# Kernel optimization log

Measured on AMD Instinct MI355X. Metric: run time of the kernel, lower is better.

## Reference

```python
import jax, jax.numpy as jnp
import numpy as np

HEAD_DIM = 128
BAND_BITS = (5, 4, 4, 3)
N_BANDS = len(BAND_BITS)
BAND = HEAD_DIM // N_BANDS  # 32
FP16_MAX = 65504.0


def _hadamard(n):
    H = np.array([[1.0]], dtype=np.float32)
    while H.shape[0] < n:
        H = np.block([[H, H], [H, -H]])
    return H


def _mobius_perm(n):
    # Mobius function mu(i) for i = 1..n via sieve
    mu = np.ones(n + 1, dtype=np.int64)
    is_prime = np.ones(n + 1, dtype=bool)
    for p in range(2, n + 1):
        if is_prime[p]:
            is_prime[2 * p::p] = False
            mu[p::p] *= -1
            sq = p * p
            if sq <= n:
                mu[sq::sq] = 0
    # stable reorder of the 0..n-1 coordinates by descending mu(i+1)
    perm = np.argsort(-mu[1:n + 1], kind='stable').astype(np.int32)
    inv = np.argsort(perm).astype(np.int32)
    return perm, inv

_H = jnp.asarray(_hadamard(HEAD_DIM))            # [128,128], symmetric, H@H = 128*I
_PERM, _INV_PERM = (jnp.asarray(p) for p in _mobius_perm(HEAD_DIM))


def _banded_quant_dequant(z):
    # z: [N, HEAD_DIM] in WHT+Mobius space. Per-row, per-band symmetric quantization.
    zb = z.reshape(-1, N_BANDS, BAND)                       # [N, 4, 32]
    qmax = jnp.asarray([2 ** (b - 1) - 1 for b in BAND_BITS], jnp.float32)  # [4]
    amax = jnp.max(jnp.abs(zb), axis=-1)                    # [N, 4]
    scale = jnp.where(amax > 0, amax / qmax, 1.0)           # [N, 4]
    q = jnp.clip(jnp.round(zb / scale[..., None]), -qmax[:, None], qmax[:, None])
    return (q * scale[..., None]).reshape(-1, HEAD_DIM)


def setup_inputs() -> dict:
    key = jax.random.key(0)
    k1, k2 = jax.random.split(key)
    x = jax.random.normal(k1, (2, 512, 5120), dtype=jnp.float32)
    W = jax.random.normal(k2, (5120, 5120), dtype=jnp.float32) * 0.02
    b = jnp.zeros((5120,), dtype=jnp.float32)
    return {"x": x, "W": W, "b": b}


def reference(x, W, b):
    # cache-miss path: linear projection (result = cross_attn proj of T5 context)
    y = jnp.einsum('bld,ed->ble', x, W) + b                 # [B, L, 5120]
    orig_shape = y.shape
    yf = y.reshape(-1, HEAD_DIM)                            # [B*L*n_heads, 128]
    # put(): WHT -> Mobius reorder -> banded quantize
    z = yf @ _H                                             # unnormalized WHT
    z = z[:, _PERM]
    z = _banded_quant_dequant(z)
    # get(): un-reorder -> inverse WHT (WHT then /head_dim) -> clamp/nan_to_num
    z = z[:, _INV_PERM]
    r = (z @ _H) / HEAD_DIM
    r = jnp.clip(r, -FP16_MAX, FP16_MAX)
    r = jnp.nan_to_num(r, nan=0.0)
    return r.reshape(orig_shape)
```

## Files before the change

### kernel.cpp

```cpp
#include <hip/hip_runtime.h>
#include <math.h>

#define HEAD 128
typedef _Float16 f16;
typedef _Float16 f16x8 __attribute__((ext_vector_type(8)));
typedef _Float16 f16x4 __attribute__((ext_vector_type(4)));
typedef float f32x4 __attribute__((ext_vector_type(4)));

constexpr int mu_of(int n) {
  int m = n, cnt = 0;
  for (int p = 2; p * p <= m; ++p) {
    if (m % p == 0) {
      m /= p; ++cnt;
      if (m % p == 0) return 0;
    }
  }
  if (m > 1) ++cnt;
  return (cnt & 1) ? -1 : 1;
}
constexpr int key_of(int idx) {
  int mu = mu_of(idx + 1);
  return mu == 1 ? 0 : (mu == 0 ? 1 : 2);
}
struct Tbl {
  int band[HEAD];
  float qm[HEAD];
};
constexpr Tbl make_tbl() {
  Tbl t{};
  constexpr float qv[4] = {15.f, 7.f, 7.f, 3.f};
  for (int p = 0; p < HEAD; ++p) {
    int kp = key_of(p);
    int rank = 0;
    for (int j = 0; j < HEAD; ++j) {
      int kj = key_of(j);
      if (kj < kp || (kj == kp && j < p)) ++rank;
    }
    t.band[p] = rank >> 5;
    t.qm[p] = qv[rank >> 5];
  }
  return t;
}
__constant__ Tbl g_tbl = make_tbl();

__global__ __launch_bounds__(256) void split64(const float* __restrict__ s,
                                               f16* __restrict__ h,
                                               f16* __restrict__ l, int n4) {
  int i = blockIdx.x * blockDim.x + threadIdx.x;
  if (i >= n4) return;
  float4 v = ((const float4*)s)[i];
  v.x *= 64.f; v.y *= 64.f; v.z *= 64.f; v.w *= 64.f;
  f16 hx = (f16)v.x, hy = (f16)v.y, hz = (f16)v.z, hw = (f16)v.w;
  f16 lx = (f16)(v.x - (float)hx);
  f16 ly = (f16)(v.y - (float)hy);
  f16 lz = (f16)(v.z - (float)hz);
  f16 lw = (f16)(v.w - (float)hw);
  f16x4 hv = {hx, hy, hz, hw};
  f16x4 lv = {lx, ly, lz, lw};
  *(f16x4*)(h + 4 * (size_t)i) = hv;
  *(f16x4*)(l + 4 * (size_t)i) = lv;
}

__device__ __forceinline__ void dma16(const f16* g, f16* l) {
  __builtin_amdgcn_global_load_lds(
      (const __attribute__((address_space(1))) unsigned int*)g,
      (__attribute__((address_space(3))) unsigned int*)l, 16, 0, 0);
}

__global__ __launch_bounds__(64) void gemm_f16split(
    const f16* __restrict__ Ah, const f16* __restrict__ Al,
    const f16* __restrict__ Bh, const f16* __restrict__ Bl,
    const float* __restrict__ bias, float* __restrict__ C,
    int M, int N, int K) {
  __shared__ f16 sAh[64 * 32];
  __shared__ f16 sAl[64 * 32];
  __shared__ f16 sBh[64 * 32];
  __shared__ f16 sBl[64 * 32];

  const int lane = threadIdx.x;
  const int m0 = blockIdx.x * 64;
  const int n0 = blockIdx.y * 64;

  const int srow = lane >> 2;
  const int scol = (lane & 3) * 8;
  const f16* gAh = Ah + (size_t)(m0 + srow) * K + scol;
  const f16* gAl = Al + (size_t)(m0 + srow) * K + scol;
  const f16* gBh = Bh + (size_t)(n0 + srow) * K + scol;
  const f16* gBl = Bl + (size_t)(n0 + srow) * K + scol;
  const size_t rstep = (size_t)16 * K;

  f32x4 acc[4][4];
#pragma unroll
  for (int i = 0; i < 4; ++i)
#pragma unroll
    for (int j = 0; j < 4; ++j) acc[i][j] = (f32x4){0.f, 0.f, 0.f, 0.f};

#pragma unroll
  for (int j = 0; j < 4; ++j) {
    dma16(gAh + j * rstep, &sAh[j * 512]);
    dma16(gAl + j * rstep, &sAl[j * 512]);
    dma16(gBh + j * rstep, &sBh[j * 512]);
    dma16(gBl + j * rstep, &sBl[j * 512]);
  }

  const int frow = lane & 15;
  const int kq = lane >> 4;
  const int fbase = frow * 32 + kq * 8;

  for (int k0 = 0; k0 < K; k0 += 32) {
    __syncthreads();
    f16x8 ah[4], al[4], bh[4], bl[4];
#pragma unroll
    for (int s = 0; s < 4; ++s) {
      ah[s] = *(const f16x8*)&sAh[s * 512 + fbase];
      al[s] = *(const f16x8*)&sAl[s * 512 + fbase];
      bh[s] = *(const f16x8*)&sBh[s * 512 + fbase];
      bl[s] = *(const f16x8*)&sBl[s * 512 + fbase];
    }
    __syncthreads();
    if (k0 + 32 < K) {
      const int kn = k0 + 32;
#pragma unroll
      for (int j = 0; j < 4; ++j) {
        dma16(gAh + kn + j * rstep, &sAh[j * 512]);
        dma16(gAl + kn + j * rstep, &sAl[j * 512]);
        dma16(gBh + kn + j * rstep, &sBh[j * 512]);
        dma16(gBl + kn + j * rstep, &sBl[j * 512]);
      }
    }
#pragma unroll
    for (int i = 0; i < 4; ++i)
#pragma unroll
      for (int j = 0; j < 4; ++j) {
        acc[i][j] = __builtin_amdgcn_mfma_f32_16x16x32_f16(ah[i], bh[j], acc[i][j], 0, 0, 0);
        acc[i][j] = __builtin_amdgcn_mfma_f32_16x16x32_f16(al[i], bh[j], acc[i][j], 0, 0, 0);
        acc[i][j] = __builtin_amdgcn_mfma_f32_16x16x32_f16(ah[i], bl[j], acc[i][j], 0, 0, 0);
      }
  }

  const float inv = 1.f / 4096.f;
#pragma unroll
  for (int j = 0; j < 4; ++j) {
    const int col = n0 + j * 16 + frow;
    const float bv = bias[col];
#pragma unroll
    for (int i = 0; i < 4; ++i) {
#pragma unroll
      for (int r = 0; r < 4; ++r) {
        const int row = m0 + i * 16 + kq * 4 + r;
        C[(size_t)row * N + col] = acc[i][j][r] * inv + bv;
      }
    }
  }
}

#define BM 128
#define BN 64
#define BKK 8
#define TM 8
#define TN 4

__global__ __launch_bounds__(256) void sgemm_nt(
    const float* __restrict__ A, const float* __restrict__ B,
    const float* __restrict__ bias, float* __restrict__ C,
    int M, int N, int K) {
  __shared__ float As[BKK][BM];
  __shared__ float Bs[BKK][BN];

  const int tid = threadIdx.x;
  const int tn = tid & 15;
  const int tm = tid >> 4;
  const int bx = blockIdx.x;
  const int by = blockIdx.y;

  const float* Ab = A + (size_t)by * BM * K;
  const float* Bb = B + (size_t)bx * BN * K;

  const int ar = tid >> 1;
  const int ak = (tid & 1) * 4;

  float acc[TM][TN];
#pragma unroll
  for (int i = 0; i < TM; ++i)
#pragma unroll
    for (int j = 0; j < TN; ++j) acc[i][j] = 0.f;

  for (int k0 = 0; k0 < K; k0 += BKK) {
    float4 av = *(const float4*)(Ab + (size_t)ar * K + k0 + ak);
    float4 bv = make_float4(0.f, 0.f, 0.f, 0.f);
    if (tid < 128) bv = *(const float4*)(Bb + (size_t)ar * K + k0 + ak);

    __syncthreads();
    As[ak + 0][ar] = av.x;
    As[ak + 1][ar] = av.y;
    As[ak + 2][ar] = av.z;
    As[ak + 3][ar] = av.w;
    if (tid < 128) {
      Bs[ak + 0][ar] = bv.x;
      Bs[ak + 1][ar] = bv.y;
      Bs[ak + 2][ar] = bv.z;
      Bs[ak + 3][ar] = bv.w;
    }
    __syncthreads();

#pragma unroll
    for (int kk = 0; kk < BKK; ++kk) {
      float a[TM], b[TN];
#pragma unroll
      for (int i = 0; i < TM; ++i) a[i] = As[kk][tm * TM + i];
#pragma unroll
      for (int j = 0; j < TN; ++j) b[j] = Bs[kk][tn * TN + j];
#pragma unroll
      for (int i = 0; i < TM; ++i)
#pragma unroll
        for (int j = 0; j < TN; ++j) acc[i][j] += a[i] * b[j];
    }
  }

  const int row0 = by * BM + tm * TM;
  const int col0 = bx * BN + tn * TN;
  float bj[TN];
#pragma unroll
  for (int j = 0; j < TN; ++j) bj[j] = bias[col0 + j];
#pragma unroll
  for (int i = 0; i < TM; ++i) {
    float4 v = make_float4(acc[i][0] + bj[0], acc[i][1] + bj[1],
                           acc[i][2] + bj[2], acc[i][3] + bj[3]);
    *(float4*)(C + (size_t)(row0 + i) * N + col0) = v;
  }
}

__device__ inline void fwht2(float& e0, float& e1, int lane) {
  float a = e0 + e1;
  float b = e0 - e1;
  e0 = a;
  e1 = b;
#pragma unroll
  for (int s = 1; s <= 32; s <<= 1) {
    float p0 = __shfl_xor(e0, s);
    float p1 = __shfl_xor(e1, s);
    bool up = (lane & s) != 0;
    e0 = up ? (p0 - e0) : (e0 + p0);
    e1 = up ? (p1 - e1) : (e1 + p1);
  }
}

__global__ __launch_bounds__(256) void hadq(const float* __restrict__ Y,
                                            float* __restrict__ O, int nrows) {
  const int lane = threadIdx.x & 63;
  const int wave = (blockIdx.x * (blockDim.x >> 6)) + (threadIdx.x >> 6);
  const int nwaves = gridDim.x * (blockDim.x >> 6);

  const int b0 = g_tbl.band[lane];
  const int b1 = g_tbl.band[lane + 64];
  const float qm0 = g_tbl.qm[lane];
  const float qm1 = g_tbl.qm[lane + 64];

  for (int row = wave; row < nrows; row += nwaves) {
    const float* y = Y + (size_t)row * HEAD;
    float e0 = y[lane];
    float e1 = y[lane + 64];

    fwht2(e0, e1, lane);

    float f0 = fabsf(e0), f1 = fabsf(e1);
    float ab0 = fmaxf(b0 == 0 ? f0 : 0.f, b1 == 0 ? f1 : 0.f);
    float ab1 = fmaxf(b0 == 1 ? f0 : 0.f, b1 == 1 ? f1 : 0.f);
    float ab2 = fmaxf(b0 == 2 ? f0 : 0.f, b1 == 2 ? f1 : 0.f);
    float ab3 = fmaxf(b0 == 3 ? f0 : 0.f, b1 == 3 ? f1 : 0.f);
#pragma unroll
    for (int s = 32; s >= 1; s >>= 1) {
      ab0 = fmaxf(ab0, __shfl_xor(ab0, s));
      ab1 = fmaxf(ab1, __shfl_xor(ab1, s));
      ab2 = fmaxf(ab2, __shfl_xor(ab2, s));
      ab3 = fmaxf(ab3, __shfl_xor(ab3, s));
    }
    float am0 = b0 == 0 ? ab0 : (b0 == 1 ? ab1 : (b0 == 2 ? ab2 : ab3));
    float am1 = b1 == 0 ? ab0 : (b1 == 1 ? ab1 : (b1 == 2 ? ab2 : ab3));

    float s0 = am0 > 0.f ? am0 / qm0 : 1.0f;
    float s1 = am1 > 0.f ? am1 / qm1 : 1.0f;

    float q0 = fminf(fmaxf(rintf(e0 / s0), -qm0), qm0);
    float q1 = fminf(fmaxf(rintf(e1 / s1), -qm1), qm1);
    e0 = q0 * s0;
    e1 = q1 * s1;

    fwht2(e0, e1, lane);
    float r0 = e0 * 0.0078125f;
    float r1 = e1 * 0.0078125f;
    if (r0 != r0) r0 = 0.f;
    if (r1 != r1) r1 = 0.f;
    r0 = fminf(fmaxf(r0, -65504.f), 65504.f);
    r1 = fminf(fmaxf(r1, -65504.f), 65504.f);

    float* o = O + (size_t)row * HEAD;
    o[lane] = r0;
    o[lane + 64] = r1;
  }
}

extern "C" void kernel_launch(void* const* d_in, const int* in_sizes, int n_in,
                              void* d_out, int out_size, void* d_ws, size_t ws_size,
                              hipStream_t stream) {
  const float* x = (const float*)d_in[0];
  const float* W = (const float*)d_in[1];
  const float* b = (const float*)d_in[2];
  float* out = (float*)d_out;

  const int N = in_sizes[2];
  const int K = N;
  const int M = in_sizes[0] / K;

  const size_t MK = (size_t)M * K;
  const size_t NK = (size_t)N * K;
  const size_t need = (MK + NK) * 2 * sizeof(f16);

  if (ws_size >= need) {
    f16* xh = (f16*)d_ws;
    f16* xl = xh + MK;
    f16* wh = xl + MK;
    f16* wl = wh + NK;

    const int n4x = (int)(MK / 4);
    const int n4w = (int)(NK / 4);
    split64<<<(n4x + 255) / 256, 256, 0, stream>>>(x, xh, xl, n4x);
    split64<<<(n4w + 255) / 256, 256, 0, stream>>>(W, wh, wl, n4w);

    dim3 grid(M / 64, N / 64);
    gemm_f16split<<<grid, 64, 0, stream>>>(xh, xl, wh, wl, b, out, M, N, K);
  } else {
    dim3 grid(N / BN, M / BM);
    sgemm_nt<<<grid, 256, 0, stream>>>(x, W, b, out, M, N, K);
  }

  const int nrows = out_size / HEAD;
  hadq<<<512, 256, 0, stream>>>(out, out, nrows);
}
```

Measured before the change: 493.3 us.

## Double-buffer LDS in split-f16 GEMM with two-stage async DMA prefetch

Replaces the single-buffer GEMM main loop with a two-buffer LDS pipeline. Tiles t+1 and t+2 are kept in flight using global_load_lds, and completion is tracked with explicit vmcnt/lgkmcnt waits instead of __syncthreads. The global addressing is remapped so each lane's DMA slot matches its MFMA fragment. The aim is to hide global-memory latency behind the MFMA work. The cost is double the LDS footprint and correctness that depends on the hand-written waitcnt accounting. It also adds a launch-bounds occupancy hint.

```diff
diff --git a/kernel.cpp b/kernel.cpp
--- a/kernel.cpp
+++ b/kernel.cpp
@@ -67,67 +67,69 @@
       (__attribute__((address_space(3))) unsigned int*)l, 16, 0, 0);
 }
 
-__global__ __launch_bounds__(64) void gemm_f16split(
+__global__ __launch_bounds__(64, 2) void gemm_f16split_db(
     const f16* __restrict__ Ah, const f16* __restrict__ Al,
     const f16* __restrict__ Bh, const f16* __restrict__ Bl,
     const float* __restrict__ bias, float* __restrict__ C,
     int M, int N, int K) {
-  __shared__ f16 sAh[64 * 32];
-  __shared__ f16 sAl[64 * 32];
-  __shared__ f16 sBh[64 * 32];
-  __shared__ f16 sBl[64 * 32];
+  __shared__ f16 lds[2][4][2048];
 
   const int lane = threadIdx.x;
   const int m0 = blockIdx.x * 64;
   const int n0 = blockIdx.y * 64;
-
-  const int srow = lane >> 2;
-  const int scol = (lane & 3) * 8;
-  const f16* gAh = Ah + (size_t)(m0 + srow) * K + scol;
-  const f16* gAl = Al + (size_t)(m0 + srow) * K + scol;
-  const f16* gBh = Bh + (size_t)(n0 + srow) * K + scol;
-  const f16* gBl = Bl + (size_t)(n0 + srow) * K + scol;
-  const size_t rstep = (size_t)16 * K;
-
-  f32x4 acc[4][4];
-#pragma unroll
-  for (int i = 0; i < 4; ++i)
-#pragma unroll
-    for (int j = 0; j < 4; ++j) acc[i][j] = (f32x4){0.f, 0.f, 0.f, 0.f};
-
-#pragma unroll
-  for (int j = 0; j < 4; ++j) {
-    dma16(gAh + j * rstep, &sAh[j * 512]);
-    dma16(gAl + j * rstep, &sAl[j * 512]);
-    dma16(gBh + j * rstep, &sBh[j * 512]);
-    dma16(gBl + j * rstep, &sBl[j * 512]);
-  }
-
   const int frow = lane & 15;
   const int kq = lane >> 4;
-  const int fbase = frow * 32 + kq * 8;
-
-  for (int k0 = 0; k0 < K; k0 += 32) {
-    __syncthreads();
+
+  const f16* g0 = Ah + (size_t)(m0 + frow) * K + kq * 8;
+  const f16* g1 = Al + (size_t)(m0 + frow) * K + kq * 8;
+  const f16* g2 = Bh + (size_t)(n0 + frow) * K + kq * 8;
+  const f16* g3 = Bl + (size_t)(n0 + frow) * K + kq * 8;
+  const size_t rstep = (size_t)16 * K;
+
+  f32x4 acc[4][4];
+#pragma unroll
+  for (int i = 0; i < 4; ++i)
+#pragma unroll
+    for (int j = 0; j < 4; ++j) acc[i][j] = (f32x4){0.f, 0.f, 0.f, 0.f};
+
+  auto stage = [&](int t, int buf) {
+    const int k0 = t * 32;
+#pragma unroll
+    for (int i = 0; i < 4; ++i) {
+      dma16(g0 + k0 + i * rstep, &lds[buf][0][i * 512]);
+      dma16(g1 + k0 + i * rstep, &lds[buf][1][i * 512]);
+      dma16(g2 + k0 + i * rstep, &lds[buf][2][i * 512]);
+      dma16(g3 + k0 + i * rstep, &lds[buf][3][i * 512]);
+    }
+  };
+
+  const int nt = K >> 5;
+  stage(0, 0);
+  stage(1, 1);
+
+  const int lb = lane * 8;
+
+  for (int t = 0; t < nt; ++t) {
+    if (t + 1 < nt) {
+      asm volatile("s_waitcnt vmcnt(16)" ::: "memory");
+    } else {
+      asm volatile("s_waitcnt vmcnt(0)" ::: "memory");
+    }
+    const int buf = t & 1;
+
     f16x8 ah[4], al[4], bh[4], bl[4];
 #pragma unroll
-    for (int s = 0; s < 4; ++s) {
-      ah[s] = *(const f16x8*)&sAh[s * 512 + fbase];
-      al[s] = *(const f16x8*)&sAl[s * 512 + fbase];
-      bh[s] = *(const f16x8*)&sBh[s * 512 + fbase];
-      bl[s] = *(const f16x8*)&sBl[s * 512 + fbase];
-    }
-    __syncthreads();
-    if (k0 + 32 < K) {
-      const int kn = k0 + 32;
-#pragma unroll
-      for (int j = 0; j < 4; ++j) {
-        dma16(gAh + kn + j * rstep, &sAh[j * 512]);
-        dma16(gAl + kn + j * rstep, &sAl[j * 512]);
-        dma16(gBh + kn + j * rstep, &sBh[j * 512]);
-        dma16(gBl + kn + j * rstep, &sBl[j * 512]);
-      }
-    }
+    for (int i = 0; i < 4; ++i) {
+      ah[i] = *(const f16x8*)&lds[buf][0][i * 512 + lb];
+      al[i] = *(const f16x8*)&lds[buf][1][i * 512 + lb];
+      bh[i] = *(const f16x8*)&lds[buf][2][i * 512 + lb];
+      bl[i] = *(const f16x8*)&lds[buf][3][i * 512 + lb];
+    }
+    asm volatile("s_waitcnt lgkmcnt(0)" ::: "memory");
+    __builtin_amdgcn_sched_barrier(0);
+
+    if (t + 2 < nt) stage(t + 2, buf);
+
 #pragma unroll
     for (int i = 0; i < 4; ++i)
 #pragma unroll
@@ -328,7 +330,7 @@
     split64<<<(n4w + 255) / 256, 256, 0, stream>>>(W, wh, wl, n4w);
 
     dim3 grid(M / 64, N / 64);
-    gemm_f16split<<<grid, 64, 0, stream>>>(xh, xl, wh, wl, b, out, M, N, K);
+    gemm_f16split_db<<<grid, 64, 0, stream>>>(xh, xl, wh, wl, b, out, M, N, K);
   } else {
     dim3 grid(N / BN, M / BM);
     sgemm_nt<<<grid, 256, 0, stream>>>(x, W, b, out, M, N, K);
```

After: 774.7 us. 57.0% more time.
